# Optimization experiments

Measured on AMD Instinct MI355X. Metric: run time of the kernel, lower is better.

## Reference

```python
import jax, jax.numpy as jnp
import numpy as np

N_VOX = 200000   # active voxels
K = 27           # 3x3x3 kernel offsets
P = 100000       # rulebook pairs per kernel offset
C_IN = 64
C_OUT = 64
BN_EPS = 1e-5


def setup_inputs() -> dict:
    key = jax.random.key(0)
    k1, k2, k3, k4, k5 = jax.random.split(key, 5)
    features = jax.random.normal(k1, (N_VOX, C_IN), dtype=jnp.float32)
    weight = jax.random.normal(k2, (K, C_IN, C_OUT), dtype=jnp.float32) * 0.05
    bias = jax.random.normal(k3, (C_OUT,), dtype=jnp.float32) * 0.05
    gamma = jnp.ones((C_OUT,), dtype=jnp.float32)
    beta = jnp.zeros((C_OUT,), dtype=jnp.float32)
    in_idx = jax.random.randint(k4, (K, P), 0, N_VOX, dtype=jnp.int32)
    out_idx = jax.random.randint(k5, (K, P), 0, N_VOX, dtype=jnp.int32)
    return {"features": features, "weight": weight, "bias": bias,
            "gamma": gamma, "beta": beta, "in_idx": in_idx, "out_idx": out_idx}


def reference(features, weight, bias, gamma, beta, in_idx, out_idx):
    # --- sparse submanifold conv: gather -> per-offset GEMM -> scatter-add ---
    gathered = features[in_idx]                         # [K, P, C_in]
    partial = jnp.einsum('kpc,kcd->kpd', gathered, weight)  # [K, P, C_out]
    out = jnp.zeros((N_VOX, C_OUT), dtype=features.dtype)
    out = out.at[out_idx.reshape(-1)].add(partial.reshape(-1, C_OUT))
    out = out + bias                                    # conv bias
    # --- BatchNorm1d (training mode: batch stats, biased variance) ---
    mean = jnp.mean(out, axis=0)
    var = jnp.mean(jnp.square(out - mean), axis=0)
    normed = (out - mean) * jax.lax.rsqrt(var + BN_EPS) * gamma + beta
    # --- ReLU ---
    return jnp.maximum(normed, 0.0)
```

## Files before the change

kernel.cpp:

```cpp
#include <hip/hip_runtime.h>
#include <hip/hip_bf16.h>

#define N_VOX 200000
#define KOFF 27
#define PPK 100000
#define C 64
#define BN_EPS 1e-5f

typedef __bf16 bf16x8 __attribute__((ext_vector_type(8)));
typedef __bf16 bf16x4 __attribute__((ext_vector_type(4)));
typedef float f32x4 __attribute__((ext_vector_type(4)));

__global__ __launch_bounds__(256)
void convert_features(const float* __restrict__ f, __bf16* __restrict__ fb)
{
    const size_t total4 = (size_t)N_VOX * C / 4;
    const size_t i = (size_t)blockIdx.x * blockDim.x + threadIdx.x;
    if (i >= total4) return;
    const float4 v = ((const float4*)f)[i];
    bf16x4 o;
    o.x = (__bf16)v.x; o.y = (__bf16)v.y; o.z = (__bf16)v.z; o.w = (__bf16)v.w;
    ((bf16x4*)fb)[i] = o;
}

__global__ __launch_bounds__(256)
void convert_weight(const float* __restrict__ w, __bf16* __restrict__ wt)
{
    const int k = blockIdx.x;
    const float* W = w + (size_t)k * C * C;
    __bf16* Wt = wt + (size_t)k * C * C;
    for (int idx = threadIdx.x; idx < C * C; idx += 256) {
        const int ci = idx >> 6, co = idx & 63;
        Wt[co * C + ci] = (__bf16)W[idx];
    }
}

__global__ __launch_bounds__(256)
void hist_kernel(const int* __restrict__ out_idx, unsigned* __restrict__ counts,
                 int k0, int npair)
{
    const int i = blockIdx.x * 256 + threadIdx.x;
    if (i < npair) {
        const int o = out_idx[(size_t)k0 * PPK + i];
        atomicAdd(&counts[o], 1u);
    }
}

__global__ __launch_bounds__(256)
void scan1(unsigned* __restrict__ counts, unsigned* __restrict__ offsets,
           unsigned* __restrict__ bsums)
{
    __shared__ unsigned sdata[256];
    const int t = threadIdx.x;
    const int base = blockIdx.x * 1024 + t * 4;
    unsigned v[4]; unsigned s = 0;
#pragma unroll
    for (int u = 0; u < 4; ++u) {
        const bool ok = (base + u < N_VOX);
        v[u] = ok ? counts[base + u] : 0u;
        if (ok) counts[base + u] = 0u;
        s += v[u];
    }
    sdata[t] = s;
    __syncthreads();
    for (int off = 1; off < 256; off <<= 1) {
        const unsigned add = (t >= off) ? sdata[t - off] : 0u;
        __syncthreads();
        sdata[t] += add;
        __syncthreads();
    }
    const unsigned incl = sdata[t];
    unsigned run = incl - s;
    if (t == 255) bsums[blockIdx.x] = incl;
#pragma unroll
    for (int u = 0; u < 4; ++u) {
        if (base + u < N_VOX) offsets[base + u] = run;
        run += v[u];
    }
}

__global__ __launch_bounds__(256)
void scan2(unsigned* __restrict__ bsums, int nb)
{
    __shared__ unsigned sdata[256];
    const int t = threadIdx.x;
    const unsigned s = (t < nb) ? bsums[t] : 0u;
    sdata[t] = s;
    __syncthreads();
    for (int off = 1; off < 256; off <<= 1) {
        const unsigned add = (t >= off) ? sdata[t - off] : 0u;
        __syncthreads();
        sdata[t] += add;
        __syncthreads();
    }
    if (t < nb) bsums[t] = sdata[t] - s;
}

__global__ __launch_bounds__(256)
void scan3(unsigned* __restrict__ offsets, const unsigned* __restrict__ bsums,
           unsigned* __restrict__ cursor)
{
    const int i = blockIdx.x * 256 + threadIdx.x;
    if (i < N_VOX) {
        const unsigned v = offsets[i] + bsums[i >> 10];
        offsets[i] = v;
        cursor[i] = v;
    }
}

__global__ __launch_bounds__(256)
void conv_scatter(const __bf16* __restrict__ featb, const __bf16* __restrict__ wtb,
                  const int* __restrict__ in_idx, const int* __restrict__ out_idx,
                  unsigned* __restrict__ cursor, __bf16* __restrict__ partial,
                  int k0)
{
    constexpr int TP = 256;
    __shared__ __bf16 sA[TP * 64];

    const int k = k0 + blockIdx.y;
    const int tile_base = blockIdx.x * TP;
    const int t = threadIdx.x;
    const int lane = t & 63;
    const int wave = t >> 6;
    const int m16 = lane & 15;
    const int quad = lane >> 4;

    const __bf16* Wt = wtb + (size_t)k * C * C;
    bf16x8 bfrag[4][2];
#pragma unroll
    for (int nt = 0; nt < 4; ++nt)
#pragma unroll
        for (int kc = 0; kc < 2; ++kc)
            bfrag[nt][kc] = *(const bf16x8*)(Wt + (nt * 16 + m16) * C + kc * 32 + quad * 8);

    unsigned my_rank = 0u;
    {
        const int pair = tile_base + t;
        if (pair < PPK) {
            const int o = out_idx[(size_t)k * PPK + pair];
            my_rank = atomicAdd(&cursor[o], 1u);
        }
    }

    const int c8 = t & 7;
    const int r0 = t >> 3;
#pragma unroll
    for (int it = 0; it < 8; ++it) {
        const int r = r0 + it * 32;
        const int pair = tile_base + r;
        const int row = (pair < PPK) ? in_idx[(size_t)k * PPK + pair] : 0;
        const float4 v = *(const float4*)(featb + (size_t)row * C + c8 * 8);
        *(float4*)(sA + r * 64 + ((c8 ^ (r0 & 7)) << 3)) = v;
    }
    __syncthreads();

    f32x4 acc[4][4] = {};
    const int mbase = wave * 64;
#pragma unroll
    for (int kc = 0; kc < 2; ++kc) {
        bf16x8 afrag[4];
#pragma unroll
        for (int mt = 0; mt < 4; ++mt)
            afrag[mt] = *(const bf16x8*)(sA + (mbase + mt * 16 + m16) * 64
                                         + ((((kc << 2) | quad) ^ (m16 & 7)) << 3));
#pragma unroll
        for (int nt = 0; nt < 4; ++nt)
#pragma unroll
            for (int mt = 0; mt < 4; ++mt)
                acc[mt][nt] = __builtin_amdgcn_mfma_f32_16x16x32_bf16(
                    afrag[mt], bfrag[nt][kc], acc[mt][nt], 0, 0, 0);
    }

#pragma unroll
    for (int mt = 0; mt < 4; ++mt) {
#pragma unroll
        for (int reg = 0; reg < 4; ++reg) {
            const int rloc = mt * 16 + quad * 4 + reg;
            const unsigned slot = __shfl(my_rank, rloc, 64);
            const int pair = tile_base + mbase + rloc;
            if (pair < PPK) {
                bf16x4 pv;
                pv.x = (__bf16)acc[mt][0][reg];
                pv.y = (__bf16)acc[mt][1][reg];
                pv.z = (__bf16)acc[mt][2][reg];
                pv.w = (__bf16)acc[mt][3][reg];
                *(bf16x4*)(partial + (size_t)slot * C + (m16 << 2)) = pv;
            }
        }
    }
}

__global__ __launch_bounds__(256)
void reduce_kernel(const __bf16* __restrict__ partial,
                   const unsigned* __restrict__ offsets,
                   float* __restrict__ out, const int first, const unsigned np)
{
    const int wave = threadIdx.x >> 6;
    const int lane = threadIdx.x & 63;
    const int e = lane >> 4;
    const int j = lane & 15;
    const int o = blockIdx.x * 4 + wave;
    if (o >= N_VOX) return;
    const unsigned beg = offsets[o];
    const unsigned end = (o + 1 < N_VOX) ? offsets[o + 1] : np;
    float a0 = 0.f, a1 = 0.f, a2 = 0.f, a3 = 0.f;
    for (unsigned s = beg + e; s < end; s += 4) {
        const bf16x4 v = *(const bf16x4*)(partial + (size_t)s * C + (j << 2));
        a0 += (float)v.x; a1 += (float)v.y; a2 += (float)v.z; a3 += (float)v.w;
    }
#pragma unroll
    for (int mask = 16; mask <= 32; mask <<= 1) {
        a0 += __shfl_xor(a0, mask, 64);
        a1 += __shfl_xor(a1, mask, 64);
        a2 += __shfl_xor(a2, mask, 64);
        a3 += __shfl_xor(a3, mask, 64);
    }
    if (e == 0) {
        float* orow = out + (size_t)o * C;
        if (first) {
            orow[j] = a0; orow[16 + j] = a1; orow[32 + j] = a2; orow[48 + j] = a3;
        } else {
            orow[j] += a0; orow[16 + j] += a1; orow[32 + j] += a2; orow[48 + j] += a3;
        }
    }
}

__global__ __launch_bounds__(256)
void conv_mfma(const __bf16* __restrict__ featb, const __bf16* __restrict__ wtb,
               const int* __restrict__ in_idx, const int* __restrict__ out_idx,
               float* __restrict__ out)
{
    constexpr int TP = 256;
    constexpr int STRIDE = 72;
    __shared__ __bf16 sA[TP * STRIDE];
    __shared__ int s_out[TP];

    const int k = blockIdx.y;
    const int tile_base = blockIdx.x * TP;
    const int t = threadIdx.x;
    const int lane = t & 63;
    const int wave = t >> 6;
    const int m16 = lane & 15;
    const int quad = lane >> 4;

    const __bf16* Wt = wtb + (size_t)k * C * C;
    bf16x8 bfrag[4][2];
#pragma unroll
    for (int nt = 0; nt < 4; ++nt)
#pragma unroll
        for (int kc = 0; kc < 2; ++kc)
            bfrag[nt][kc] = *(const bf16x8*)(Wt + (nt * 16 + m16) * C + kc * 32 + quad * 8);

    {
        const int pair = tile_base + t;
        s_out[t] = (pair < PPK) ? out_idx[(size_t)k * PPK + pair] : 0;
    }

    const int c8 = t & 7;
    const int r0 = t >> 3;
#pragma unroll
    for (int it = 0; it < 8; ++it) {
        const int r = r0 + it * 32;
        const int pair = tile_base + r;
        const int row = (pair < PPK) ? in_idx[(size_t)k * PPK + pair] : 0;
        const float4 v = *(const float4*)(featb + (size_t)row * C + c8 * 8);
        *(float4*)(sA + r * STRIDE + c8 * 8) = v;
    }
    __syncthreads();

    f32x4 acc[4][4] = {};
    const int mbase = wave * 64;
#pragma unroll
    for (int kc = 0; kc < 2; ++kc) {
        bf16x8 afrag[4];
#pragma unroll
        for (int mt = 0; mt < 4; ++mt)
            afrag[mt] = *(const bf16x8*)(sA + (mbase + mt * 16 + m16) * STRIDE + kc * 32 + quad * 8);
#pragma unroll
        for (int nt = 0; nt < 4; ++nt)
#pragma unroll
            for (int mt = 0; mt < 4; ++mt)
                acc[mt][nt] = __builtin_amdgcn_mfma_f32_16x16x32_bf16(
                    afrag[mt], bfrag[nt][kc], acc[mt][nt], 0, 0, 0);
    }

#pragma unroll
    for (int mt = 0; mt < 4; ++mt) {
#pragma unroll
        for (int reg = 0; reg < 4; ++reg) {
            const int r = mbase + mt * 16 + quad * 4 + reg;
            const int pair = tile_base + r;
            if (pair < PPK) {
                const int o = s_out[r];
                float* orow = out + (size_t)o * C + m16;
#pragma unroll
                for (int nt = 0; nt < 4; ++nt)
                    unsafeAtomicAdd(orow + nt * 16, acc[mt][nt][reg]);
            }
        }
    }
}

__global__ __launch_bounds__(256)
void stats_kernel(const float* __restrict__ out,
                  float* __restrict__ stats,
                  int rows_per_block)
{
    __shared__ float ssum[256];
    __shared__ float ssq[256];
    const int c   = threadIdx.x & 63;
    const int sub = threadIdx.x >> 6;
    const int row0 = blockIdx.x * rows_per_block;
    const int row1 = min(row0 + rows_per_block, N_VOX);
    float s = 0.f, q = 0.f;
    for (int r = row0 + sub; r < row1; r += 4) {
        const float v = out[(size_t)r * C + c];
        s += v;
        q += v * v;
    }
    ssum[threadIdx.x] = s;
    ssq[threadIdx.x]  = q;
    __syncthreads();
    if (sub == 0) {
        s = ssum[c] + ssum[64 + c] + ssum[128 + c] + ssum[192 + c];
        q = ssq[c]  + ssq[64 + c]  + ssq[128 + c]  + ssq[192 + c];
        unsafeAtomicAdd(&stats[c], s);
        unsafeAtomicAdd(&stats[64 + c], q);
    }
}

__global__ void finalize_params(const float* __restrict__ stats,
                                const float* __restrict__ gamma,
                                const float* __restrict__ beta,
                                float* __restrict__ ss)
{
    const int c = threadIdx.x;
    const float inv_n = 1.0f / (float)N_VOX;
    const float mean  = stats[c] * inv_n;
    const float var   = stats[64 + c] * inv_n - mean * mean;
    const float scale = rsqrtf(var + BN_EPS) * gamma[c];
    ss[c]      = scale;
    ss[64 + c] = beta[c] - mean * scale;
}

__global__ __launch_bounds__(256)
void norm_kernel(float* __restrict__ out, const float* __restrict__ ss)
{
    const size_t total4 = (size_t)N_VOX * C / 4;
    const size_t idx = (size_t)blockIdx.x * blockDim.x + threadIdx.x;
    if (idx >= total4) return;
    const int c4 = (int)(idx & 15);
    float4 v = ((const float4*)out)[idx];
    const float4 sc = ((const float4*)ss)[c4];
    const float4 sh = ((const float4*)(ss + 64))[c4];
    v.x = fmaxf(v.x * sc.x + sh.x, 0.f);
    v.y = fmaxf(v.y * sc.y + sh.y, 0.f);
    v.z = fmaxf(v.z * sc.z + sh.z, 0.f);
    v.w = fmaxf(v.w * sc.w + sh.w, 0.f);
    ((float4*)out)[idx] = v;
}

static inline size_t align_up(size_t x) { return (x + 255) & ~(size_t)255; }

extern "C" void kernel_launch(void* const* d_in, const int* in_sizes, int n_in,
                              void* d_out, int out_size, void* d_ws, size_t ws_size,
                              hipStream_t stream)
{
    const float* features = (const float*)d_in[0];
    const float* weight   = (const float*)d_in[1];
    const float* gamma    = (const float*)d_in[3];
    const float* beta     = (const float*)d_in[4];
    const int*   in_idx   = (const int*)d_in[5];
    const int*   out_idx  = (const int*)d_in[6];
    float* out = (float*)d_out;

    char* base = (char*)d_ws;
    size_t off = 0;
    __bf16* featb = (__bf16*)(base + off); off += align_up((size_t)N_VOX * C * 2);
    __bf16* wtb   = (__bf16*)(base + off); off += align_up((size_t)KOFF * C * C * 2);
    float*  stats = (float*)(base + off);  off += align_up(128 * 4);
    float*  ss    = (float*)(base + off);  off += align_up(128 * 4);
    unsigned* counts  = (unsigned*)(base + off); off += align_up((size_t)N_VOX * 4);
    unsigned* offsets = (unsigned*)(base + off); off += align_up((size_t)N_VOX * 4);
    unsigned* cursor  = (unsigned*)(base + off); off += align_up((size_t)N_VOX * 4);
    unsigned* bsums   = (unsigned*)(base + off); off += align_up(256 * 4);
    const size_t fixed = off;

    int g_cap = 0;
    if (ws_size > fixed)
        g_cap = (int)((ws_size - fixed) / ((size_t)PPK * 128));
    if (g_cap > 9) g_cap = 9;

    hipMemsetAsync(stats, 0, 128 * sizeof(float), stream);

    const size_t total4 = (size_t)N_VOX * C / 4;
    convert_features<<<(int)((total4 + 255) / 256), 256, 0, stream>>>(features, featb);
    convert_weight<<<KOFF, 256, 0, stream>>>(weight, wtb);

    if (g_cap >= 2) {
        const int G = (KOFF + g_cap - 1) / g_cap;
        __bf16* partial = (__bf16*)(base + off);
        const int gbase_sz = KOFF / G, rem = KOFF % G;
        hipMemsetAsync(counts, 0, (size_t)N_VOX * 4, stream);
        int k0 = 0;
        for (int ci = 0; ci < G; ++ci) {
            const int g = gbase_sz + (ci < rem ? 1 : 0);
            const int np = g * PPK;
            hist_kernel<<<(np + 255) / 256, 256, 0, stream>>>(out_idx, counts, k0, np);
            scan1<<<(N_VOX + 1023) / 1024, 256, 0, stream>>>(counts, offsets, bsums);
            scan2<<<1, 256, 0, stream>>>(bsums, (N_VOX + 1023) / 1024);
            scan3<<<(N_VOX + 255) / 256, 256, 0, stream>>>(offsets, bsums, cursor);
            dim3 cgrid((PPK + 255) / 256, g);
            conv_scatter<<<cgrid, 256, 0, stream>>>(featb, wtb, in_idx, out_idx,
                                                    cursor, partial, k0);
            reduce_kernel<<<(N_VOX + 3) / 4, 256, 0, stream>>>(partial, offsets, out,
                                                               ci == 0 ? 1 : 0,
                                                               (unsigned)np);
            k0 += g;
        }
    } else {
        hipMemsetAsync(out, 0, (size_t)N_VOX * C * sizeof(float), stream);
        dim3 cgrid((PPK + 255) / 256, KOFF);
        conv_mfma<<<cgrid, 256, 0, stream>>>(featb, wtb, in_idx, out_idx, out);
    }

    const int rpb = (N_VOX + 511) / 512;
    stats_kernel<<<512, 256, 0, stream>>>(out, stats, rpb);

    finalize_params<<<1, 64, 0, stream>>>(stats, gamma, beta, ss);

    norm_kernel<<<(int)((total4 + 255) / 256), 256, 0, stream>>>(out, ss);
}
```

Measured before the change: 699.9 us.

## Precompute per-pair scatter slots in histogram pass and enlarge offset groups

```diff
diff --git a/kernel.cpp b/kernel.cpp
--- a/kernel.cpp
+++ b/kernel.cpp
@@ -37,12 +37,12 @@
 
 __global__ __launch_bounds__(256)
 void hist_kernel(const int* __restrict__ out_idx, unsigned* __restrict__ counts,
-                 int k0, int npair)
+                 unsigned* __restrict__ slot, int k0, int npair)
 {
     const int i = blockIdx.x * 256 + threadIdx.x;
     if (i < npair) {
         const int o = out_idx[(size_t)k0 * PPK + i];
-        atomicAdd(&counts[o], 1u);
+        slot[i] = atomicAdd(&counts[o], 1u);
     }
 }
 
@@ -97,27 +97,34 @@
 }
 
 __global__ __launch_bounds__(256)
-void scan3(unsigned* __restrict__ offsets, const unsigned* __restrict__ bsums,
-           unsigned* __restrict__ cursor)
+void scan3(unsigned* __restrict__ offsets, const unsigned* __restrict__ bsums)
 {
     const int i = blockIdx.x * 256 + threadIdx.x;
-    if (i < N_VOX) {
-        const unsigned v = offsets[i] + bsums[i >> 10];
-        offsets[i] = v;
-        cursor[i] = v;
+    if (i < N_VOX) offsets[i] += bsums[i >> 10];
+}
+
+__global__ __launch_bounds__(256)
+void slot_fill(const int* __restrict__ out_idx,
+               const unsigned* __restrict__ offsets,
+               unsigned* __restrict__ slot, int k0, int npair)
+{
+    const int i = blockIdx.x * 256 + threadIdx.x;
+    if (i < npair) {
+        const int o = out_idx[(size_t)k0 * PPK + i];
+        slot[i] += offsets[o];
     }
 }
 
 __global__ __launch_bounds__(256)
 void conv_scatter(const __bf16* __restrict__ featb, const __bf16* __restrict__ wtb,
-                  const int* __restrict__ in_idx, const int* __restrict__ out_idx,
-                  unsigned* __restrict__ cursor, __bf16* __restrict__ partial,
-                  int k0)
+                  const int* __restrict__ in_idx, const unsigned* __restrict__ slot,
+                  __bf16* __restrict__ partial, int k0)
 {
     constexpr int TP = 256;
     __shared__ __bf16 sA[TP * 64];
 
-    const int k = k0 + blockIdx.y;
+    const int kloc = blockIdx.y;
+    const int k = k0 + kloc;
     const int tile_base = blockIdx.x * TP;
     const int t = threadIdx.x;
     const int lane = t & 63;
@@ -125,6 +132,12 @@
     const int m16 = lane & 15;
     const int quad = lane >> 4;
 
+    unsigned my_slot = 0u;
+    {
+        const int pair = tile_base + t;
+        if (pair < PPK) my_slot = slot[(size_t)kloc * PPK + pair];
+    }
+
     const __bf16* Wt = wtb + (size_t)k * C * C;
     bf16x8 bfrag[4][2];
 #pragma unroll
@@ -132,15 +145,6 @@
 #pragma unroll
         for (int kc = 0; kc < 2; ++kc)
             bfrag[nt][kc] = *(const bf16x8*)(Wt + (nt * 16 + m16) * C + kc * 32 + quad * 8);
-
-    unsigned my_rank = 0u;
-    {
-        const int pair = tile_base + t;
-        if (pair < PPK) {
-            const int o = out_idx[(size_t)k * PPK + pair];
-            my_rank = atomicAdd(&cursor[o], 1u);
-        }
-    }
 
     const int c8 = t & 7;
     const int r0 = t >> 3;
@@ -176,7 +180,7 @@
 #pragma unroll
         for (int reg = 0; reg < 4; ++reg) {
             const int rloc = mt * 16 + quad * 4 + reg;
-            const unsigned slot = __shfl(my_rank, rloc, 64);
+            const unsigned s = __shfl(my_slot, rloc, 64);
             const int pair = tile_base + mbase + rloc;
             if (pair < PPK) {
                 bf16x4 pv;
@@ -184,7 +188,7 @@
                 pv.y = (__bf16)acc[mt][1][reg];
                 pv.z = (__bf16)acc[mt][2][reg];
                 pv.w = (__bf16)acc[mt][3][reg];
-                *(bf16x4*)(partial + (size_t)slot * C + (m16 << 2)) = pv;
+                *(bf16x4*)(partial + (size_t)s * C + (m16 << 2)) = pv;
             }
         }
     }
@@ -199,28 +203,29 @@
     const int lane = threadIdx.x & 63;
     const int e = lane >> 4;
     const int j = lane & 15;
-    const int o = blockIdx.x * 4 + wave;
-    if (o >= N_VOX) return;
-    const unsigned beg = offsets[o];
-    const unsigned end = (o + 1 < N_VOX) ? offsets[o + 1] : np;
-    float a0 = 0.f, a1 = 0.f, a2 = 0.f, a3 = 0.f;
-    for (unsigned s = beg + e; s < end; s += 4) {
-        const bf16x4 v = *(const bf16x4*)(partial + (size_t)s * C + (j << 2));
-        a0 += (float)v.x; a1 += (float)v.y; a2 += (float)v.z; a3 += (float)v.w;
-    }
-#pragma unroll
-    for (int mask = 16; mask <= 32; mask <<= 1) {
-        a0 += __shfl_xor(a0, mask, 64);
-        a1 += __shfl_xor(a1, mask, 64);
-        a2 += __shfl_xor(a2, mask, 64);
-        a3 += __shfl_xor(a3, mask, 64);
-    }
-    if (e == 0) {
-        float* orow = out + (size_t)o * C;
-        if (first) {
-            orow[j] = a0; orow[16 + j] = a1; orow[32 + j] = a2; orow[48 + j] = a3;
-        } else {
-            orow[j] += a0; orow[16 + j] += a1; orow[32 + j] += a2; orow[48 + j] += a3;
+    const int stride = gridDim.x * 4;
+    for (int o = blockIdx.x * 4 + wave; o < N_VOX; o += stride) {
+        const unsigned beg = offsets[o];
+        const unsigned end = (o + 1 < N_VOX) ? offsets[o + 1] : np;
+        float a0 = 0.f, a1 = 0.f, a2 = 0.f, a3 = 0.f;
+        for (unsigned s = beg + e; s < end; s += 4) {
+            const bf16x4 v = *(const bf16x4*)(partial + (size_t)s * C + (j << 2));
+            a0 += (float)v.x; a1 += (float)v.y; a2 += (float)v.z; a3 += (float)v.w;
+        }
+#pragma unroll
+        for (int mask = 16; mask <= 32; mask <<= 1) {
+            a0 += __shfl_xor(a0, mask, 64);
+            a1 += __shfl_xor(a1, mask, 64);
+            a2 += __shfl_xor(a2, mask, 64);
+            a3 += __shfl_xor(a3, mask, 64);
+        }
+        if (e == 0) {
+            float* orow = out + (size_t)o * C;
+            if (first) {
+                orow[j] = a0; orow[16 + j] = a1; orow[32 + j] = a2; orow[48 + j] = a3;
+            } else {
+                orow[j] += a0; orow[16 + j] += a1; orow[32 + j] += a2; orow[48 + j] += a3;
+            }
         }
     }
 }
@@ -382,14 +387,13 @@
     float*  ss    = (float*)(base + off);  off += align_up(128 * 4);
     unsigned* counts  = (unsigned*)(base + off); off += align_up((size_t)N_VOX * 4);
     unsigned* offsets = (unsigned*)(base + off); off += align_up((size_t)N_VOX * 4);
-    unsigned* cursor  = (unsigned*)(base + off); off += align_up((size_t)N_VOX * 4);
     unsigned* bsums   = (unsigned*)(base + off); off += align_up(256 * 4);
     const size_t fixed = off;
 
     int g_cap = 0;
     if (ws_size > fixed)
-        g_cap = (int)((ws_size - fixed) / ((size_t)PPK * 128));
-    if (g_cap > 9) g_cap = 9;
+        g_cap = (int)((ws_size - fixed) / ((size_t)PPK * 132));
+    if (g_cap > KOFF) g_cap = KOFF;
 
     hipMemsetAsync(stats, 0, 128 * sizeof(float), stream);
 
@@ -399,23 +403,24 @@
 
     if (g_cap >= 2) {
         const int G = (KOFF + g_cap - 1) / g_cap;
-        __bf16* partial = (__bf16*)(base + off);
+        const int gmax = (KOFF + G - 1) / G;
+        unsigned* slot = (unsigned*)(base + off);
+        __bf16* partial = (__bf16*)(base + off + align_up((size_t)gmax * PPK * 4));
         const int gbase_sz = KOFF / G, rem = KOFF % G;
         hipMemsetAsync(counts, 0, (size_t)N_VOX * 4, stream);
         int k0 = 0;
         for (int ci = 0; ci < G; ++ci) {
             const int g = gbase_sz + (ci < rem ? 1 : 0);
             const int np = g * PPK;
-            hist_kernel<<<(np + 255) / 256, 256, 0, stream>>>(out_idx, counts, k0, np);
+            hist_kernel<<<(np + 255) / 256, 256, 0, stream>>>(out_idx, counts, slot, k0, np);
             scan1<<<(N_VOX + 1023) / 1024, 256, 0, stream>>>(counts, offsets, bsums);
             scan2<<<1, 256, 0, stream>>>(bsums, (N_VOX + 1023) / 1024);
-            scan3<<<(N_VOX + 255) / 256, 256, 0, stream>>>(offsets, bsums, cursor);
+            scan3<<<(N_VOX + 255) / 256, 256, 0, stream>>>(offsets, bsums);
+            slot_fill<<<(np + 255) / 256, 256, 0, stream>>>(out_idx, offsets, slot, k0, np);
             dim3 cgrid((PPK + 255) / 256, g);
-            conv_scatter<<<cgrid, 256, 0, stream>>>(featb, wtb, in_idx, out_idx,
-                                                    cursor, partial, k0);
-            reduce_kernel<<<(N_VOX + 3) / 4, 256, 0, stream>>>(partial, offsets, out,
-                                                               ci == 0 ? 1 : 0,
-                                                               (unsigned)np);
+            conv_scatter<<<cgrid, 256, 0, stream>>>(featb, wtb, in_idx, slot, partial, k0);
+            reduce_kernel<<<1024, 256, 0, stream>>>(partial, offsets, out,
+                                                    ci == 0 ? 1 : 0, (unsigned)np);
             k0 += g;
         }
     } else {
```

Result: faster. 660.6 us (-5.6%).

## Bucket pairs by output block and fuse conv, scatter-add and BN stats in LDS

Applied to the files above, without the earlier changes.

```diff
diff --git a/kernel.cpp b/kernel.cpp
--- a/kernel.cpp
+++ b/kernel.cpp
@@ -6,6 +6,11 @@
 #define PPK 100000
 #define C 64
 #define BN_EPS 1e-5f
+
+#define NBLK 782
+#define NKEY (NBLK * KOFF)
+#define NPAIR (KOFF * PPK)
+#define PADMAX (NPAIR + NKEY * 15)
 
 typedef __bf16 bf16x8 __attribute__((ext_vector_type(8)));
 typedef __bf16 bf16x4 __attribute__((ext_vector_type(4)));
@@ -36,192 +41,166 @@
 }
 
 __global__ __launch_bounds__(256)
-void hist_kernel(const int* __restrict__ out_idx, unsigned* __restrict__ counts,
-                 int k0, int npair)
+void hist2(const int* __restrict__ out_idx, unsigned* __restrict__ counts)
 {
     const int i = blockIdx.x * 256 + threadIdx.x;
-    if (i < npair) {
-        const int o = out_idx[(size_t)k0 * PPK + i];
-        atomicAdd(&counts[o], 1u);
-    }
-}
-
-__global__ __launch_bounds__(256)
-void scan1(unsigned* __restrict__ counts, unsigned* __restrict__ offsets,
-           unsigned* __restrict__ bsums)
+    if (i < NPAIR) {
+        const int o = out_idx[i];
+        const int k = i / PPK;
+        atomicAdd(&counts[(o >> 8) * KOFF + k], 1u);
+    }
+}
+
+__global__ __launch_bounds__(256)
+void scan_pad(const unsigned* __restrict__ counts, unsigned* __restrict__ soff,
+              unsigned* __restrict__ cursor)
 {
     __shared__ unsigned sdata[256];
     const int t = threadIdx.x;
-    const int base = blockIdx.x * 1024 + t * 4;
-    unsigned v[4]; unsigned s = 0;
-#pragma unroll
-    for (int u = 0; u < 4; ++u) {
-        const bool ok = (base + u < N_VOX);
-        v[u] = ok ? counts[base + u] : 0u;
-        if (ok) counts[base + u] = 0u;
-        s += v[u];
+    const int CH = (NKEY + 255) / 256;
+    const int i0 = t * CH;
+    unsigned s = 0;
+    for (int j = 0; j < CH; ++j) {
+        const int i = i0 + j;
+        if (i < NKEY) s += ((counts[i] + 15u) & ~15u);
     }
     sdata[t] = s;
     __syncthreads();
     for (int off = 1; off < 256; off <<= 1) {
-        const unsigned add = (t >= off) ? sdata[t - off] : 0u;
+        const unsigned a = (t >= off) ? sdata[t - off] : 0u;
         __syncthreads();
-        sdata[t] += add;
+        sdata[t] += a;
         __syncthreads();
     }
-    const unsigned incl = sdata[t];
-    unsigned run = incl - s;
-    if (t == 255) bsums[blockIdx.x] = incl;
-#pragma unroll
-    for (int u = 0; u < 4; ++u) {
-        if (base + u < N_VOX) offsets[base + u] = run;
-        run += v[u];
-    }
-}
-
-__global__ __launch_bounds__(256)
-void scan2(unsigned* __restrict__ bsums, int nb)
-{
-    __shared__ unsigned sdata[256];
+    unsigned run = sdata[t] - s;
+    for (int j = 0; j < CH; ++j) {
+        const int i = i0 + j;
+        if (i < NKEY) {
+            soff[i] = run;
+            cursor[i] = run;
+            run += ((counts[i] + 15u) & ~15u);
+        }
+    }
+    if (t == 255) soff[NKEY] = run;
+}
+
+__global__ __launch_bounds__(256)
+void fill_kernel(unsigned* __restrict__ sorted_in, unsigned char* __restrict__ sorted_ol)
+{
+    const int i = blockIdx.x * 256 + threadIdx.x;
+    if (i < PADMAX) { sorted_in[i] = N_VOX; sorted_ol[i] = 0; }
+}
+
+__global__ __launch_bounds__(256)
+void scatter_kernel(const int* __restrict__ out_idx, const int* __restrict__ in_idx,
+                    unsigned* __restrict__ cursor, unsigned* __restrict__ sorted_in,
+                    unsigned char* __restrict__ sorted_ol)
+{
+    const int i = blockIdx.x * 256 + threadIdx.x;
+    if (i < NPAIR) {
+        const int o = out_idx[i];
+        const int k = i / PPK;
+        const unsigned pos = atomicAdd(&cursor[(o >> 8) * KOFF + k], 1u);
+        sorted_in[pos] = (unsigned)in_idx[i];
+        sorted_ol[pos] = (unsigned char)(o & 255);
+    }
+}
+
+__global__ __launch_bounds__(512)
+void conv_fused(const __bf16* __restrict__ featb, const __bf16* __restrict__ wtb,
+                const unsigned* __restrict__ sorted_in,
+                const unsigned char* __restrict__ sorted_ol,
+                const unsigned* __restrict__ soff,
+                float* __restrict__ out, float* __restrict__ stats)
+{
+    __shared__ float sout[256 * C];
+    __shared__ unsigned skoff[KOFF + 1];
+    __shared__ float sstat[1024];
+
+    const int b = blockIdx.x;
     const int t = threadIdx.x;
-    const unsigned s = (t < nb) ? bsums[t] : 0u;
-    sdata[t] = s;
-    __syncthreads();
-    for (int off = 1; off < 256; off <<= 1) {
-        const unsigned add = (t >= off) ? sdata[t - off] : 0u;
-        __syncthreads();
-        sdata[t] += add;
-        __syncthreads();
-    }
-    if (t < nb) bsums[t] = sdata[t] - s;
-}
-
-__global__ __launch_bounds__(256)
-void scan3(unsigned* __restrict__ offsets, const unsigned* __restrict__ bsums,
-           unsigned* __restrict__ cursor)
-{
-    const int i = blockIdx.x * 256 + threadIdx.x;
-    if (i < N_VOX) {
-        const unsigned v = offsets[i] + bsums[i >> 10];
-        offsets[i] = v;
-        cursor[i] = v;
-    }
-}
-
-__global__ __launch_bounds__(256)
-void conv_scatter(const __bf16* __restrict__ featb, const __bf16* __restrict__ wtb,
-                  const int* __restrict__ in_idx, const int* __restrict__ out_idx,
-                  unsigned* __restrict__ cursor, __bf16* __restrict__ partial,
-                  int k0)
-{
-    constexpr int TP = 256;
-    __shared__ __bf16 sA[TP * 64];
-
-    const int k = k0 + blockIdx.y;
-    const int tile_base = blockIdx.x * TP;
-    const int t = threadIdx.x;
+
+    {
+        f32x4* p = (f32x4*)sout;
+        for (int i = t; i < 256 * C / 4; i += 512) p[i] = (f32x4){0.f, 0.f, 0.f, 0.f};
+    }
+    if (t < KOFF + 1) skoff[t] = soff[b * KOFF + t];
+    __syncthreads();
+
+    const int wave = t >> 6;
     const int lane = t & 63;
-    const int wave = t >> 6;
     const int m16 = lane & 15;
     const int quad = lane >> 4;
 
-    const __bf16* Wt = wtb + (size_t)k * C * C;
-    bf16x8 bfrag[4][2];
-#pragma unroll
-    for (int nt = 0; nt < 4; ++nt)
-#pragma unroll
-        for (int kc = 0; kc < 2; ++kc)
-            bfrag[nt][kc] = *(const bf16x8*)(Wt + (nt * 16 + m16) * C + kc * 32 + quad * 8);
-
-    unsigned my_rank = 0u;
-    {
-        const int pair = tile_base + t;
-        if (pair < PPK) {
-            const int o = out_idx[(size_t)k * PPK + pair];
-            my_rank = atomicAdd(&cursor[o], 1u);
-        }
-    }
-
-    const int c8 = t & 7;
-    const int r0 = t >> 3;
-#pragma unroll
-    for (int it = 0; it < 8; ++it) {
-        const int r = r0 + it * 32;
-        const int pair = tile_base + r;
-        const int row = (pair < PPK) ? in_idx[(size_t)k * PPK + pair] : 0;
-        const float4 v = *(const float4*)(featb + (size_t)row * C + c8 * 8);
-        *(float4*)(sA + r * 64 + ((c8 ^ (r0 & 7)) << 3)) = v;
-    }
-    __syncthreads();
-
-    f32x4 acc[4][4] = {};
-    const int mbase = wave * 64;
-#pragma unroll
-    for (int kc = 0; kc < 2; ++kc) {
-        bf16x8 afrag[4];
-#pragma unroll
-        for (int mt = 0; mt < 4; ++mt)
-            afrag[mt] = *(const bf16x8*)(sA + (mbase + mt * 16 + m16) * 64
-                                         + ((((kc << 2) | quad) ^ (m16 & 7)) << 3));
+    int ctile = 0;
+    for (int k = 0; k < KOFF; ++k) {
+        const unsigned rb = skoff[k];
+        const int ntk = (int)((skoff[k + 1] - rb) >> 4);
+        int lt = (wave - ctile) & 7;
+        ctile += ntk;
+        if (lt >= ntk) continue;
+
+        const __bf16* Wt = wtb + (size_t)k * C * C;
+        bf16x8 bfrag[4][2];
 #pragma unroll
         for (int nt = 0; nt < 4; ++nt)
 #pragma unroll
-            for (int mt = 0; mt < 4; ++mt)
-                acc[mt][nt] = __builtin_amdgcn_mfma_f32_16x16x32_bf16(
-                    afrag[mt], bfrag[nt][kc], acc[mt][nt], 0, 0, 0);
-    }
-
-#pragma unroll
-    for (int mt = 0; mt < 4; ++mt) {
-#pragma unroll
-        for (int reg = 0; reg < 4; ++reg) {
-            const int rloc = mt * 16 + quad * 4 + reg;
-            const unsigned slot = __shfl(my_rank, rloc, 64);
-            const int pair = tile_base + mbase + rloc;
-            if (pair < PPK) {
-                bf16x4 pv;
-                pv.x = (__bf16)acc[mt][0][reg];
-                pv.y = (__bf16)acc[mt][1][reg];
-                pv.z = (__bf16)acc[mt][2][reg];
-                pv.w = (__bf16)acc[mt][3][reg];
-                *(bf16x4*)(partial + (size_t)slot * C + (m16 << 2)) = pv;
+            for (int kc = 0; kc < 2; ++kc)
+                bfrag[nt][kc] = *(const bf16x8*)(Wt + (nt * 16 + m16) * C + kc * 32 + quad * 8);
+
+        unsigned rowA = sorted_in[rb + ((unsigned)lt << 4) + m16];
+        for (; lt < ntk; ) {
+            const unsigned tb = rb + ((unsigned)lt << 4);
+            const __bf16* fr = featb + (size_t)rowA * C + quad * 8;
+            const bf16x8 a0 = *(const bf16x8*)(fr);
+            const bf16x8 a1 = *(const bf16x8*)(fr + 32);
+            const int ol0 = sorted_ol[tb + quad * 4 + 0];
+            const int ol1 = sorted_ol[tb + quad * 4 + 1];
+            const int ol2 = sorted_ol[tb + quad * 4 + 2];
+            const int ol3 = sorted_ol[tb + quad * 4 + 3];
+
+            lt += 8;
+            if (lt < ntk)
+                rowA = sorted_in[rb + ((unsigned)lt << 4) + m16];
+
+            f32x4 acc[4] = {};
+#pragma unroll
+            for (int nt = 0; nt < 4; ++nt) {
+                acc[nt] = __builtin_amdgcn_mfma_f32_16x16x32_bf16(a0, bfrag[nt][0], acc[nt], 0, 0, 0);
+                acc[nt] = __builtin_amdgcn_mfma_f32_16x16x32_bf16(a1, bfrag[nt][1], acc[nt], 0, 0, 0);
+            }
+#pragma unroll
+            for (int nt = 0; nt < 4; ++nt) {
+                atomicAdd(&sout[ol0 * C + nt * 16 + m16], acc[nt][0]);
+                atomicAdd(&sout[ol1 * C + nt * 16 + m16], acc[nt][1]);
+                atomicAdd(&sout[ol2 * C + nt * 16 + m16], acc[nt][2]);
+                atomicAdd(&sout[ol3 * C + nt * 16 + m16], acc[nt][3]);
             }
         }
     }
-}
-
-__global__ __launch_bounds__(256)
-void reduce_kernel(const __bf16* __restrict__ partial,
-                   const unsigned* __restrict__ offsets,
-                   float* __restrict__ out, const int first, const unsigned np)
-{
-    const int wave = threadIdx.x >> 6;
-    const int lane = threadIdx.x & 63;
-    const int e = lane >> 4;
-    const int j = lane & 15;
-    const int o = blockIdx.x * 4 + wave;
-    if (o >= N_VOX) return;
-    const unsigned beg = offsets[o];
-    const unsigned end = (o + 1 < N_VOX) ? offsets[o + 1] : np;
-    float a0 = 0.f, a1 = 0.f, a2 = 0.f, a3 = 0.f;
-    for (unsigned s = beg + e; s < end; s += 4) {
-        const bf16x4 v = *(const bf16x4*)(partial + (size_t)s * C + (j << 2));
-        a0 += (float)v.x; a1 += (float)v.y; a2 += (float)v.z; a3 += (float)v.w;
-    }
-#pragma unroll
-    for (int mask = 16; mask <= 32; mask <<= 1) {
-        a0 += __shfl_xor(a0, mask, 64);
-        a1 += __shfl_xor(a1, mask, 64);
-        a2 += __shfl_xor(a2, mask, 64);
-        a3 += __shfl_xor(a3, mask, 64);
-    }
-    if (e == 0) {
-        float* orow = out + (size_t)o * C;
-        if (first) {
-            orow[j] = a0; orow[16 + j] = a1; orow[32 + j] = a2; orow[48 + j] = a3;
-        } else {
-            orow[j] += a0; orow[16 + j] += a1; orow[32 + j] += a2; orow[48 + j] += a3;
+    __syncthreads();
+
+    const int row_cap = min(256, N_VOX - b * 256);
+    const int c = t & 63;
+    const int r0 = t >> 6;
+    float s = 0.f, q = 0.f;
+    for (int r = r0; r < row_cap; r += 8) {
+        const float v = sout[r * C + c];
+        out[((size_t)(b * 256 + r)) * C + c] = v;
+        s += v; q += v * v;
+    }
+    sstat[t] = s;
+    sstat[512 + t] = q;
+    __syncthreads();
+    if (t < C) {
+        float ssum = 0.f, sq = 0.f;
+#pragma unroll
+        for (int u = 0; u < 8; ++u) {
+            ssum += sstat[u * 64 + t];
+            sq   += sstat[512 + u * 64 + t];
         }
+        unsafeAtomicAdd(&stats[t], ssum);
+        unsafeAtomicAdd(&stats[64 + t], sq);
     }
 }
 
@@ -376,20 +355,16 @@
 
     char* base = (char*)d_ws;
     size_t off = 0;
-    __bf16* featb = (__bf16*)(base + off); off += align_up((size_t)N_VOX * C * 2);
+    __bf16* featb = (__bf16*)(base + off); off += align_up((size_t)(N_VOX + 1) * C * 2);
     __bf16* wtb   = (__bf16*)(base + off); off += align_up((size_t)KOFF * C * C * 2);
     float*  stats = (float*)(base + off);  off += align_up(128 * 4);
     float*  ss    = (float*)(base + off);  off += align_up(128 * 4);
-    unsigned* counts  = (unsigned*)(base + off); off += align_up((size_t)N_VOX * 4);
-    unsigned* offsets = (unsigned*)(base + off); off += align_up((size_t)N_VOX * 4);
-    unsigned* cursor  = (unsigned*)(base + off); off += align_up((size_t)N_VOX * 4);
-    unsigned* bsums   = (unsigned*)(base + off); off += align_up(256 * 4);
-    const size_t fixed = off;
-
-    int g_cap = 0;
-    if (ws_size > fixed)
-        g_cap = (int)((ws_size - fixed) / ((size_t)PPK * 128));
-    if (g_cap > 9) g_cap = 9;
+    unsigned* counts  = (unsigned*)(base + off); off += align_up((size_t)NKEY * 4);
+    unsigned* soff    = (unsigned*)(base + off); off += align_up((size_t)(NKEY + 1) * 4);
+    unsigned* cursor  = (unsigned*)(base + off); off += align_up((size_t)NKEY * 4);
+    unsigned* sorted_in = (unsigned*)(base + off); off += align_up((size_t)PADMAX * 4);
+    unsigned char* sorted_ol = (unsigned char*)(base + off); off += align_up((size_t)PADMAX);
+    const size_t needed = off;
 
     hipMemsetAsync(stats, 0, 128 * sizeof(float), stream);
 
@@ -397,35 +372,23 @@
     convert_features<<<(int)((total4 + 255) / 256), 256, 0, stream>>>(features, featb);
     convert_weight<<<KOFF, 256, 0, stream>>>(weight, wtb);
 
-    if (g_cap >= 2) {
-        const int G = (KOFF + g_cap - 1) / g_cap;
-        __bf16* partial = (__bf16*)(base + off);
-        const int gbase_sz = KOFF / G, rem = KOFF % G;
-        hipMemsetAsync(counts, 0, (size_t)N_VOX * 4, stream);
-        int k0 = 0;
-        for (int ci = 0; ci < G; ++ci) {
-            const int g = gbase_sz + (ci < rem ? 1 : 0);
-            const int np = g * PPK;
-            hist_kernel<<<(np + 255) / 256, 256, 0, stream>>>(out_idx, counts, k0, np);
-            scan1<<<(N_VOX + 1023) / 1024, 256, 0, stream>>>(counts, offsets, bsums);
-            scan2<<<1, 256, 0, stream>>>(bsums, (N_VOX + 1023) / 1024);
-            scan3<<<(N_VOX + 255) / 256, 256, 0, stream>>>(offsets, bsums, cursor);
-            dim3 cgrid((PPK + 255) / 256, g);
-            conv_scatter<<<cgrid, 256, 0, stream>>>(featb, wtb, in_idx, out_idx,
-                                                    cursor, partial, k0);
-            reduce_kernel<<<(N_VOX + 3) / 4, 256, 0, stream>>>(partial, offsets, out,
-                                                               ci == 0 ? 1 : 0,
-                                                               (unsigned)np);
-            k0 += g;
-        }
+    if (ws_size >= needed) {
+        hipMemsetAsync(counts, 0, (size_t)NKEY * 4, stream);
+        hipMemsetAsync(featb + (size_t)N_VOX * C, 0, C * 2, stream);
+        hist2<<<(NPAIR + 255) / 256, 256, 0, stream>>>(out_idx, counts);
+        scan_pad<<<1, 256, 0, stream>>>(counts, soff, cursor);
+        fill_kernel<<<(PADMAX + 255) / 256, 256, 0, stream>>>(sorted_in, sorted_ol);
+        scatter_kernel<<<(NPAIR + 255) / 256, 256, 0, stream>>>(out_idx, in_idx, cursor,
+                                                                sorted_in, sorted_ol);
+        conv_fused<<<NBLK, 512, 0, stream>>>(featb, wtb, sorted_in, sorted_ol,
+                                             soff, out, stats);
     } else {
         hipMemsetAsync(out, 0, (size_t)N_VOX * C * sizeof(float), stream);
         dim3 cgrid((PPK + 255) / 256, KOFF);
         conv_mfma<<<cgrid, 256, 0, stream>>>(featb, wtb, in_idx, out_idx, out);
-    }
-
-    const int rpb = (N_VOX + 511) / 512;
-    stats_kernel<<<512, 256, 0, stream>>>(out, stats, rpb);
+        const int rpb = (N_VOX + 511) / 512;
+        stats_kernel<<<512, 256, 0, stream>>>(out, stats, rpb);
+    }
 
     finalize_params<<<1, 64, 0, stream>>>(stats, gamma, beta, ss);
 
```

Result: slower. 1.695 ms (+142.2%).
